# Performance work log

Measured on AMD Instinct MI355X. Metric: run time of the kernel, lower is better.

Reference implementation:

```python
import jax, jax.numpy as jnp
import numpy as np

B, LQ, LF, NW, NFR, E, D, V = 4, 128, 64, 2, 8, 128, 128, 64


def _project(x, W, b):
    # torch Emb_Projection('linear'): Linear then zero-row mask
    y = x @ W + b
    m = 1.0 - jnp.all(y == 0, axis=-1, keepdims=True).astype(y.dtype)
    return y * m


def setup_inputs() -> dict:
    key = jax.random.key(0)
    ks = jax.random.split(key, 12)
    s = lambda k, shape, fan: jax.random.normal(k, shape, jnp.float32) / np.sqrt(fan)
    return {
        "query": jax.random.normal(ks[0], (B, LQ, E), jnp.float32),
        "fragment": jax.random.normal(ks[1], (B, NW, NFR, LF, E), jnp.float32),
        "query_mask": jnp.ones((B, LQ), jnp.float32),
        "fragment_mask": jnp.ones((B, NW, NFR, LF), jnp.float32),
        # learned params (stored [in, out]; torch Linear is x @ W.T with W [out,in])
        "proj_W": s(ks[2], (E, D), E),
        "proj_b": jnp.zeros((D,), jnp.float32),
        "self_att_W": s(ks[3], (NW, D), D),   # n_way Linear(D,1,bias=False)
        "q_att_W": s(ks[4], (D, V), D),
        "f_att_W": s(ks[5], (D, V), D),
        "qf_att_W": s(ks[6], (D, V), D),
        "gate_w": s(ks[7], (V,), V),          # value_gate: Linear(V,1,bias=False)
        "val_w": s(ks[8], (V,), V),           # value_att:  Linear(V,1,bias=False)
    }


def reference(query, fragment, query_mask, fragment_mask, proj_W, proj_b,
              self_att_W, q_att_W, f_att_W, qf_att_W, gate_w, val_w):
    query = _project(query, proj_W, proj_b)          # [B,Lq,D]
    fragment = _project(fragment, proj_W, proj_b)    # [B,NW,NFR,Lf,D]

    # (1) fragment self-attention -> frag_code
    logits = jnp.einsum('bwfld,wd->bwfl', fragment, self_att_W)   # per-way Linear(D,1)
    e = jnp.exp(logits) * fragment_mask
    frag_self_att = e / (e.sum(-1, keepdims=True) + 1e-7)          # [B,NW,NFR,Lf]
    frag_code = (fragment * frag_self_att[..., None]).sum(-2)     # [B,NW,NFR,D]

    # (2) query-to-fragment attention
    frag_r = fragment.reshape(fragment.shape[0], -1, fragment.shape[-2], fragment.shape[-1])  # [B,NF,Lf,D]
    qr = query[:, None]                                            # [B,1,Lq,D]
    q_att = qr @ q_att_W                                           # [B,1,Lq,V]
    f_att = frag_r @ f_att_W                                       # [B,NF,Lf,V]
    # large broadcast product [B,NF,Lf,Lq,D] then project to V
    qf = (qr[:, :, None, :, :] * frag_r[:, :, :, None, :]) @ qf_att_W  # [B,NF,Lf,Lq,V]
    qf = q_att[:, :, None] + f_att[:, :, :, None] + qf
    qf = qf.max(axis=-3)                                           # max over Lf -> [B,NF,Lq,V]

    qf_gate = jax.nn.sigmoid(qf @ gate_w) * query_mask[:, None]    # [B,NF,Lq]
    e2 = jnp.exp(qf @ val_w) * query_mask[:, None]
    qf_norm = e2 / (e2.sum(-1, keepdims=True) + 1e-7)              # [B,NF,Lq]

    query_code = (qr * qf_norm[..., None]).sum(axis=2)             # [B,NF,D]
    query_code = query_code.reshape(frag_code.shape)               # [B,NW,NFR,D]
    return frag_code, query_code, frag_self_att, qf_gate, query
```

## Files before the change

kernel.cpp:

```cpp
#include <hip/hip_runtime.h>
#include <hip/hip_bf16.h>

#define B_   4
#define LQ_  128
#define LF_  64
#define NW_  2
#define NFR_ 8
#define E_   128
#define D_   128
#define V_   64
#define NWF_ (NW_*NFR_)

using bf16 = __hip_bfloat16;
typedef unsigned short u16;
typedef unsigned int   u32;
typedef __attribute__((ext_vector_type(8))) short  bf16x8;
typedef __attribute__((ext_vector_type(4))) float  f32x4;
typedef __attribute__((ext_vector_type(4))) u32    u32x4;

#define WS_PWT   0
#define WS_QAT   8192
#define WS_W3T   12288
#define WS_WFT   16384
#define WS_E2    20480
#define WS_QPB   28672

#define OUT_FRAGCODE  0
#define OUT_QUERYCODE 8192
#define OUT_SELFATT   16384
#define OUT_QFGATE    20480
#define OUT_QUERY     28672

#define L_FP   0
#define L_QP   16384
#define L_FA   24576
#define L_QAT  33792
#define L_SAW  38400
#define L_ATT  38912
#define L_RED  39168
#define L_TOT  41216

__device__ __forceinline__ float us2f(u16 v) { return __uint_as_float((u32)v << 16); }
__device__ __forceinline__ float lo2f(u32 v) { return __uint_as_float(v << 16); }
__device__ __forceinline__ float hi2f(u32 v) { return __uint_as_float(v & 0xffff0000u); }
__device__ __forceinline__ u16 f2b_raw(float f) {
    u32 u = __float_as_uint(f);
    return (u16)((u + 0x7fffu + ((u >> 16) & 1u)) >> 16);
}
__device__ __forceinline__ u32 pk2(float hi, float lo) {
    return __builtin_amdgcn_perm(__float_as_uint(hi), __float_as_uint(lo), 0x07060302u);
}
template<bool BF> __device__ __forceinline__ float LD(const void* p, int i) {
    return BF ? us2f(((const u16*)p)[i]) : ((const float*)p)[i];
}
template<bool BF> __device__ __forceinline__ void ST(void* p, int i, float v) {
    if (BF) ((u16*)p)[i] = f2b_raw(v); else ((float*)p)[i] = v;
}
template<bool BF> __device__ __forceinline__ u16 LDB(const void* p, int i) {
    return BF ? ((const u16*)p)[i] : f2b_raw(((const float*)p)[i]);
}
__device__ __forceinline__ bool is_bf(const void* qmask) {
    return ((const u16*)qmask)[0] == 0x3F80u;
}
template<bool BF>
__device__ __forceinline__ bf16x8 loadA(const void* x, int row, int kt, int quad) {
    int off = row * 128 + kt * 32 + quad * 8;
    if (BF) return *(const bf16x8*)((const u16*)x + off);
    f32x4 a = *(const f32x4*)((const float*)x + off);
    f32x4 c = *(const f32x4*)((const float*)x + off + 4);
    u32x4 av;
    av.x = pk2(a.y, a.x); av.y = pk2(a.w, a.z);
    av.z = pk2(c.y, c.x); av.w = pk2(c.w, c.z);
    return __builtin_bit_cast(bf16x8, av);
}

template<bool BF>
__device__ __forceinline__ void prep_body(const void* src, u16* dst, u16* stg,
                                          int N, int k0)
{
    int t = threadIdx.x, st = N + 1, total = 32 * N;
    for (int i = t; i < total; i += 256) {
        int k = i / N, v = i % N;
        stg[k * st + v] = LDB<BF>(src, (k0 + k) * N + v);
    }
    __syncthreads();
    for (int j = t; j < total; j += 256) {
        int n = j >> 5, kk = j & 31;
        dst[n * 128 + k0 + kk] = stg[kk * st + n];
    }
}
__global__ __launch_bounds__(256) void k_prep(
    const void* projW, const void* qattW, const void* qfW, const void* fattW,
    const void* qmask, float* ws)
{
    __shared__ u16 stg[32 * 129];
    int mat = blockIdx.x >> 2, kq = blockIdx.x & 3;
    const void* src = (mat == 0) ? projW : (mat == 1) ? qattW : (mat == 2) ? qfW : fattW;
    u16* dst = (u16*)(ws + ((mat == 0) ? WS_PWT : (mat == 1) ? WS_QAT : (mat == 2) ? WS_W3T : WS_WFT));
    int N = (mat == 0) ? 128 : 64;
    if (is_bf(qmask)) prep_body<true >(src, dst, stg, N, kq * 32);
    else              prep_body<false>(src, dst, stg, N, kq * 32);
}

template<bool BF>
__device__ __forceinline__ void main_body(
    const void* query, const void* fragment, const void* qmask, const void* fmask,
    const void* projB, const void* saW, const void* gatew, const void* valw,
    float* ws, void* out, char* smem)
{
    u16*   s_fp  = (u16*)(smem + L_FP);
    u16*   s_qp  = (u16*)(smem + L_QP);
    u16*   s_fa  = (u16*)(smem + L_FA);
    u16*   s_qat = (u16*)(smem + L_QAT);
    float* s_saw = (float*)(smem + L_SAW);
    float* s_att = (float*)(smem + L_ATT);
    float* s_red = (float*)(smem + L_RED);

    int bx = blockIdx.x;
    int qt = bx >> 6, bwf = bx & 63, b = bwf >> 4;
    int t = threadIdx.x, lane = t & 63, w = t >> 6;
    int m = lane & 15, quad = lane >> 4;
    int sk = (m & 7) << 3;
    const u16* pwt = (const u16*)(ws + WS_PWT);
    const u16* qatw = (const u16*)(ws + WS_QAT);
    const u16* w3t = (const u16*)(ws + WS_W3T);
    const u16* wft = (const u16*)(ws + WS_WFT);
    bool do_fragatt = (qt == (bwf & 3));
    bool do_export  = ((bwf & 15) == 0);

    if (w < 4) {
        bf16x8 afr[4];
        #pragma unroll
        for (int kt = 0; kt < 4; ++kt)
            afr[kt] = loadA<BF>(fragment, bwf * 64 + w * 16 + m, kt, quad);
        #pragma unroll
        for (int nt = 0; nt < 8; ++nt) {
            int n = nt * 16 + m;
            float bv = LD<BF>(projB, n);
            f32x4 acc = (f32x4){bv, bv, bv, bv};
            #pragma unroll
            for (int kt = 0; kt < 4; ++kt) {
                bf16x8 bw = *(const bf16x8*)(pwt + n * 128 + kt * 32 + quad * 8);
                acc = __builtin_amdgcn_mfma_f32_16x16x32_bf16(afr[kt], bw, acc, 0, 0, 0);
            }
            #pragma unroll
            for (int rr = 0; rr < 4; ++rr) {
                int row = w * 16 + quad * 4 + rr;
                s_fp[row * 128 + (n ^ ((row & 7) << 3))] = f2b_raw(acc[rr]);
            }
        }
    } else if (w < 6) {
        int q0 = (w - 4) * 16;
        bf16x8 afq[4];
        #pragma unroll
        for (int kt = 0; kt < 4; ++kt)
            afq[kt] = loadA<BF>(query, b * 128 + qt * 32 + q0 + m, kt, quad);
        #pragma unroll
        for (int nt = 0; nt < 8; ++nt) {
            int n = nt * 16 + m;
            float bv = LD<BF>(projB, n);
            f32x4 acc = (f32x4){bv, bv, bv, bv};
            #pragma unroll
            for (int kt = 0; kt < 4; ++kt) {
                bf16x8 bw = *(const bf16x8*)(pwt + n * 128 + kt * 32 + quad * 8);
                acc = __builtin_amdgcn_mfma_f32_16x16x32_bf16(afq[kt], bw, acc, 0, 0, 0);
            }
            #pragma unroll
            for (int rr = 0; rr < 4; ++rr) {
                int row = q0 + quad * 4 + rr;
                s_qp[row * 128 + (n ^ ((row & 7) << 3))] = f2b_raw(acc[rr]);
            }
        }
    }
    __syncthreads();

    if (w < 4) {
        bf16x8 afa[4];
        #pragma unroll
        for (int kt = 0; kt < 4; ++kt)
            afa[kt] = *(const bf16x8*)&s_fp[(w * 16 + m) * 128 + ((kt * 32 + quad * 8) ^ sk)];
        #pragma unroll
        for (int vt = 0; vt < 4; ++vt) {
            f32x4 a0 = (f32x4){0.f, 0.f, 0.f, 0.f};
            #pragma unroll
            for (int kt = 0; kt < 4; ++kt) {
                bf16x8 wk = *(const bf16x8*)(wft + (vt * 16 + m) * 128 + kt * 32 + quad * 8);
                a0 = __builtin_amdgcn_mfma_f32_16x16x32_bf16(afa[kt], wk, a0, 0, 0, 0);
            }
            #pragma unroll
            for (int r = 0; r < 4; ++r)
                s_fa[(w * 16 + quad * 4 + r) * 72 + vt * 16 + m] = f2b_raw(a0[r]);
        }
    } else if (w < 6) {
        int q0 = (w - 4) * 16;
        bf16x8 aq[4];
        #pragma unroll
        for (int kt = 0; kt < 4; ++kt)
            aq[kt] = *(const bf16x8*)&s_qp[(q0 + m) * 128 + ((kt * 32 + quad * 8) ^ sk)];
        #pragma unroll
        for (int vt = 0; vt < 4; ++vt) {
            f32x4 a0 = (f32x4){0.f, 0.f, 0.f, 0.f};
            #pragma unroll
            for (int kt = 0; kt < 4; ++kt) {
                bf16x8 bk = *(const bf16x8*)(qatw + (vt * 16 + m) * 128 + kt * 32 + quad * 8);
                a0 = __builtin_amdgcn_mfma_f32_16x16x32_bf16(aq[kt], bk, a0, 0, 0, 0);
            }
            #pragma unroll
            for (int r = 0; r < 4; ++r)
                s_qat[(q0 + quad * 4 + r) * 72 + vt * 16 + m] = f2b_raw(a0[r]);
        }
    }
    __syncthreads();

    int qsub = w & 1, lhalf = (w >> 1) & 1, vhalf = (w >> 2) & 1;
    bf16x8 w3f[2][4];
    #pragma unroll
    for (int i = 0; i < 2; ++i)
        #pragma unroll
        for (int kt = 0; kt < 4; ++kt)
            w3f[i][kt] = *(const bf16x8*)(w3t + ((vhalf * 2 + i) * 16 + m) * 128 + kt * 32 + quad * 8);
    float qpreg[4][8];
    {
        #pragma unroll
        for (int kt = 0; kt < 4; ++kt) {
            bf16x8 aq2 = *(const bf16x8*)&s_qp[(qsub * 16 + m) * 128 + ((kt * 32 + quad * 8) ^ sk)];
            u32x4 uv = __builtin_bit_cast(u32x4, aq2);
            qpreg[kt][0] = lo2f(uv.x); qpreg[kt][1] = hi2f(uv.x);
            qpreg[kt][2] = lo2f(uv.y); qpreg[kt][3] = hi2f(uv.y);
            qpreg[kt][4] = lo2f(uv.z); qpreg[kt][5] = hi2f(uv.z);
            qpreg[kt][6] = lo2f(uv.w); qpreg[kt][7] = hi2f(uv.w);
        }
    }
    float mx[2][4];
    #pragma unroll
    for (int i = 0; i < 2; ++i)
        #pragma unroll
        for (int r = 0; r < 4; ++r) mx[i][r] = -1e30f;

    int lbase = lhalf * 32;
    #pragma unroll 2
    for (int li = 0; li < 32; ++li) {
        int l = lbase + li;
        int sw = (l & 7) << 3;
        bf16x8 af[4];
        #pragma unroll
        for (int kt = 0; kt < 4; ++kt) {
            u32x4 fv = *(const u32x4*)&s_fp[l * 128 + ((kt * 32 + quad * 8) ^ sw)];
            u32x4 av;
            av.x = pk2(qpreg[kt][1] * hi2f(fv.x), qpreg[kt][0] * lo2f(fv.x));
            av.y = pk2(qpreg[kt][3] * hi2f(fv.y), qpreg[kt][2] * lo2f(fv.y));
            av.z = pk2(qpreg[kt][5] * hi2f(fv.z), qpreg[kt][4] * lo2f(fv.z));
            av.w = pk2(qpreg[kt][7] * hi2f(fv.w), qpreg[kt][6] * lo2f(fv.w));
            af[kt] = __builtin_bit_cast(bf16x8, av);
        }
        #pragma unroll
        for (int i = 0; i < 2; ++i) {
            float fa = us2f(s_fa[l * 72 + (vhalf * 2 + i) * 16 + m]);
            f32x4 acc = (f32x4){fa, fa, fa, fa};
            #pragma unroll
            for (int kt = 0; kt < 4; ++kt)
                acc = __builtin_amdgcn_mfma_f32_16x16x32_bf16(af[kt], w3f[i][kt], acc, 0, 0, 0);
            #pragma unroll
            for (int r = 0; r < 4; ++r) mx[i][r] = fmaxf(mx[i][r], acc[r]);
        }
    }
    __syncthreads();
    #pragma unroll
    for (int i = 0; i < 2; ++i)
        #pragma unroll
        for (int r = 0; r < 4; ++r)
            s_fa[(lhalf * 32 + qsub * 16 + quad * 4 + r) * 72 + (vhalf * 2 + i) * 16 + m] = f2b_raw(mx[i][r]);
    __syncthreads();

    {
        int q = t >> 4, vg = t & 15;
        int gq = qt * 32 + q;
        float gp = 0.f, ep = 0.f;
        #pragma unroll
        for (int jj = 0; jj < 4; ++jj) {
            int v = vg * 4 + jj;
            float mval = fmaxf(us2f(s_fa[q * 72 + v]), us2f(s_fa[(32 + q) * 72 + v]));
            float qf = mval + us2f(s_qat[q * 72 + v]);
            gp += qf * LD<BF>(gatew, v);
            ep += qf * LD<BF>(valw, v);
        }
        #pragma unroll
        for (int off = 1; off <= 8; off <<= 1) {
            gp += __shfl_xor(gp, off, 64);
            ep += __shfl_xor(ep, off, 64);
        }
        if (vg == 0) {
            float qm = LD<BF>(qmask, b * 128 + gq);
            float g = (1.0f / (1.0f + expf(-gp))) * qm;
            ST<BF>(out, OUT_QFGATE + bwf * LQ_ + gq, g);
            ws[WS_E2 + bwf * 128 + gq] = expf(ep) * qm;
        }
    }

    if (do_export) {
        u16* qpb = (u16*)(ws + WS_QPB);
        #pragma unroll
        for (int it = 0; it < 8; ++it) {
            int i = t + 512 * it;
            int row = i >> 7, col = i & 127;
            u16 raw = s_qp[row * 128 + (col ^ ((row & 7) << 3))];
            int gr = b * 128 + qt * 32 + row;
            ST<BF>(out, OUT_QUERY + gr * 128 + col, us2f(raw));
            qpb[gr * 128 + col] = raw;
        }
    }

    if (do_fragatt) {
        if (t < 128) s_saw[t] = LD<BF>(saW, ((bwf >> 3) & 1) * 128 + t);
        __syncthreads();
        {
            int l = t >> 3, j8 = t & 7;
            int swz = (l & 7) << 3;
            float p = 0.f;
            #pragma unroll
            for (int seg = 0; seg < 2; ++seg) {
                int koff = j8 * 16 + seg * 8;
                u32x4 fv = *(const u32x4*)&s_fp[l * 128 + (koff ^ swz)];
                const float* swp = &s_saw[koff];
                p += lo2f(fv.x) * swp[0] + hi2f(fv.x) * swp[1]
                   + lo2f(fv.y) * swp[2] + hi2f(fv.y) * swp[3]
                   + lo2f(fv.z) * swp[4] + hi2f(fv.z) * swp[5]
                   + lo2f(fv.w) * swp[6] + hi2f(fv.w) * swp[7];
            }
            p += __shfl_xor(p, 1, 64);
            p += __shfl_xor(p, 2, 64);
            p += __shfl_xor(p, 4, 64);
            if (j8 == 0) s_att[l] = expf(p) * LD<BF>(fmask, bwf * LF_ + l);
        }
        __syncthreads();
        if (t < 64) {
            float e = s_att[t], s = e;
            #pragma unroll
            for (int off = 1; off <= 32; off <<= 1) s += __shfl_xor(s, off, 64);
            float nrm = e / (s + 1e-7f);
            s_att[t] = nrm;
            ST<BF>(out, OUT_SELFATT + bwf * LF_ + t, nrm);
        }
        __syncthreads();
        {
            int d = t & 127, grp = t >> 7;
            float fc = 0.f;
            #pragma unroll
            for (int li2 = 0; li2 < 16; ++li2) {
                int l2 = grp * 16 + li2;
                fc += us2f(s_fp[l2 * 128 + (d ^ ((l2 & 7) << 3))]) * s_att[l2];
            }
            s_red[grp * 128 + d] = fc;
        }
        __syncthreads();
        if (t < 128)
            ST<BF>(out, OUT_FRAGCODE + bwf * D_ + t,
                   s_red[t] + s_red[128 + t] + s_red[256 + t] + s_red[384 + t]);
    }
}
__global__ __launch_bounds__(512, 4) void k_main(
    const void* query, const void* fragment, const void* qmask, const void* fmask,
    const void* projB, const void* saW, const void* gatew, const void* valw,
    float* ws, void* out)
{
    __shared__ char smem[L_TOT];
    if (is_bf(qmask))
        main_body<true >(query, fragment, qmask, fmask, projB, saW, gatew, valw, ws, out, smem);
    else
        main_body<false>(query, fragment, qmask, fmask, projB, saW, gatew, valw, ws, out, smem);
}

template<bool BF>
__device__ __forceinline__ void qcode_body(const float* ws, void* out,
                                           u16* s_q, float* s_n, float* s_part)
{
    int bwf = blockIdx.x, b = bwf >> 4, t = threadIdx.x;
    {
        const u32* src = (const u32*)((const u16*)(ws + WS_QPB) + (size_t)b * 16384);
        u32* dst = (u32*)s_q;
        #pragma unroll
        for (int it = 0; it < 64; ++it) dst[t + 128 * it] = src[t + 128 * it];
    }
    float e = ws[WS_E2 + bwf * 128 + t];
    float s = e;
    #pragma unroll
    for (int off = 1; off <= 32; off <<= 1) s += __shfl_xor(s, off, 64);
    if ((t & 63) == 0) s_part[t >> 6] = s;
    __syncthreads();
    float tot = s_part[0] + s_part[1] + 1e-7f;
    s_n[t] = e / tot;
    __syncthreads();
    float qc = 0.f;
    #pragma unroll 8
    for (int q = 0; q < 128; ++q)
        qc += us2f(s_q[q * 128 + t]) * s_n[q];
    ST<BF>(out, OUT_QUERYCODE + bwf * D_ + t, qc);
}
__global__ __launch_bounds__(128) void k_qcode(const void* qmask, const float* ws, void* out)
{
    __shared__ u16 s_q[128 * 128];
    __shared__ float s_n[128];
    __shared__ float s_part[2];
    if (is_bf(qmask)) qcode_body<true >(ws, out, s_q, s_n, s_part);
    else              qcode_body<false>(ws, out, s_q, s_n, s_part);
}

extern "C" void kernel_launch(void* const* d_in, const int* in_sizes, int n_in,
                              void* d_out, int out_size, void* d_ws, size_t ws_size,
                              hipStream_t stream)
{
    const void* query    = d_in[0];
    const void* fragment = d_in[1];
    const void* qmask    = d_in[2];
    const void* fmask    = d_in[3];
    const void* projW    = d_in[4];
    const void* projB    = d_in[5];
    const void* saW      = d_in[6];
    const void* qattW    = d_in[7];
    const void* fattW    = d_in[8];
    const void* qfW      = d_in[9];
    const void* gatew    = d_in[10];
    const void* valw     = d_in[11];
    float* ws = (float*)d_ws;

    hipLaunchKernelGGL(k_prep, dim3(16), dim3(256), 0, stream,
                       projW, qattW, qfW, fattW, qmask, ws);
    hipLaunchKernelGGL(k_main, dim3(256), dim3(512), 0, stream,
                       query, fragment, qmask, fmask, projB, saW, gatew, valw, ws, d_out);
    hipLaunchKernelGGL(k_qcode, dim3(B_ * NWF_), dim3(128), 0, stream,
                       qmask, ws, d_out);
}
```

Before: 110.9 us.

## Fuse query_code reduction into main kernel via atomic partial sums

Removes the separate k_qcode launch. Each main block now computes an unnormalized partial query_code over its 32 query rows plus the partial exp sum, and adds both atomically into a workspace accumulator that k_prep zeroes. A per-fragment counter picks the last of the four blocks, which normalizes and writes the output. This saves a kernel launch and the round trip of the projected query and e2 through global memory, at the cost of atomics, an extra block-wide sync and a threadfence in the main kernel.

```diff
diff --git a/kernel.cpp b/kernel.cpp
--- a/kernel.cpp
+++ b/kernel.cpp
@@ -22,8 +22,9 @@
 #define WS_QAT   8192
 #define WS_W3T   12288
 #define WS_WFT   16384
-#define WS_E2    20480
-#define WS_QPB   28672
+#define WS_ACC   20480
+#define WS_CNT   28928
+#define WS_ZTOT  8512
 
 #define OUT_FRAGCODE  0
 #define OUT_QUERYCODE 8192
@@ -38,7 +39,10 @@
 #define L_SAW  38400
 #define L_ATT  38912
 #define L_RED  39168
-#define L_TOT  41216
+#define L_E2   41216
+#define L_FLG  41344
+#define L_ES   41348
+#define L_TOT  41360
 
 __device__ __forceinline__ float us2f(u16 v) { return __uint_as_float((u32)v << 16); }
 __device__ __forceinline__ float lo2f(u32 v) { return __uint_as_float(v << 16); }
@@ -94,7 +98,14 @@
     const void* qmask, float* ws)
 {
     __shared__ u16 stg[32 * 129];
-    int mat = blockIdx.x >> 2, kq = blockIdx.x & 3;
+    int bx = blockIdx.x;
+    {
+        int per = (WS_ZTOT + 15) / 16;
+        int base = WS_ACC + bx * per;
+        for (int i = threadIdx.x; i < per; i += 256)
+            if (bx * per + i < WS_ZTOT) ws[base + i] = 0.f;
+    }
+    int mat = bx >> 2, kq = bx & 3;
     const void* src = (mat == 0) ? projW : (mat == 1) ? qattW : (mat == 2) ? qfW : fattW;
     u16* dst = (u16*)(ws + ((mat == 0) ? WS_PWT : (mat == 1) ? WS_QAT : (mat == 2) ? WS_W3T : WS_WFT));
     int N = (mat == 0) ? 128 : 64;
@@ -115,6 +126,9 @@
     float* s_saw = (float*)(smem + L_SAW);
     float* s_att = (float*)(smem + L_ATT);
     float* s_red = (float*)(smem + L_RED);
+    float* s_e2  = (float*)(smem + L_E2);
+    int*   s_flg = (int*)(smem + L_FLG);
+    float* s_es  = (float*)(smem + L_ES);
 
     int bx = blockIdx.x;
     int qt = bx >> 6, bwf = bx & 63, b = bwf >> 4;
@@ -293,12 +307,41 @@
             float qm = LD<BF>(qmask, b * 128 + gq);
             float g = (1.0f / (1.0f + expf(-gp))) * qm;
             ST<BF>(out, OUT_QFGATE + bwf * LQ_ + gq, g);
-            ws[WS_E2 + bwf * 128 + gq] = expf(ep) * qm;
-        }
+            s_e2[q] = expf(ep) * qm;
+        }
+    }
+    __syncthreads();
+
+    {
+        float* acc = ws + WS_ACC + bwf * 132;
+        if (t < 128) {
+            float qc = 0.f;
+            #pragma unroll
+            for (int q = 0; q < 32; ++q)
+                qc += us2f(s_qp[q * 128 + (t ^ ((q & 7) << 3))]) * s_e2[q];
+            atomicAdd(&acc[t], qc);
+        } else if (t == 128) {
+            float es = 0.f;
+            #pragma unroll
+            for (int q = 0; q < 32; ++q) es += s_e2[q];
+            atomicAdd(&acc[128], es);
+        }
+        __threadfence();
+        __syncthreads();
+        if (t == 0) *s_flg = atomicAdd((int*)(ws + WS_CNT) + bwf, 1);
+        __syncthreads();
+        bool last = (*s_flg == 3);
+        float qcv = 0.f;
+        if (last) {
+            if (t < 128) qcv = atomicAdd(&acc[t], 0.f);
+            if (t == 0)  *s_es = atomicAdd(&acc[128], 0.f);
+        }
+        __syncthreads();
+        if (last && t < 128)
+            ST<BF>(out, OUT_QUERYCODE + bwf * D_ + t, qcv / (*s_es + 1e-7f));
     }
 
     if (do_export) {
-        u16* qpb = (u16*)(ws + WS_QPB);
         #pragma unroll
         for (int it = 0; it < 8; ++it) {
             int i = t + 512 * it;
@@ -306,7 +349,6 @@
             u16 raw = s_qp[row * 128 + (col ^ ((row & 7) << 3))];
             int gr = b * 128 + qt * 32 + row;
             ST<BF>(out, OUT_QUERY + gr * 128 + col, us2f(raw));
-            qpb[gr * 128 + col] = raw;
         }
     }
 
@@ -368,41 +410,6 @@
         main_body<true >(query, fragment, qmask, fmask, projB, saW, gatew, valw, ws, out, smem);
     else
         main_body<false>(query, fragment, qmask, fmask, projB, saW, gatew, valw, ws, out, smem);
-}
-
-template<bool BF>
-__device__ __forceinline__ void qcode_body(const float* ws, void* out,
-                                           u16* s_q, float* s_n, float* s_part)
-{
-    int bwf = blockIdx.x, b = bwf >> 4, t = threadIdx.x;
-    {
-        const u32* src = (const u32*)((const u16*)(ws + WS_QPB) + (size_t)b * 16384);
-        u32* dst = (u32*)s_q;
-        #pragma unroll
-        for (int it = 0; it < 64; ++it) dst[t + 128 * it] = src[t + 128 * it];
-    }
-    float e = ws[WS_E2 + bwf * 128 + t];
-    float s = e;
-    #pragma unroll
-    for (int off = 1; off <= 32; off <<= 1) s += __shfl_xor(s, off, 64);
-    if ((t & 63) == 0) s_part[t >> 6] = s;
-    __syncthreads();
-    float tot = s_part[0] + s_part[1] + 1e-7f;
-    s_n[t] = e / tot;
-    __syncthreads();
-    float qc = 0.f;
-    #pragma unroll 8
-    for (int q = 0; q < 128; ++q)
-        qc += us2f(s_q[q * 128 + t]) * s_n[q];
-    ST<BF>(out, OUT_QUERYCODE + bwf * D_ + t, qc);
-}
-__global__ __launch_bounds__(128) void k_qcode(const void* qmask, const float* ws, void* out)
-{
-    __shared__ u16 s_q[128 * 128];
-    __shared__ float s_n[128];
-    __shared__ float s_part[2];
-    if (is_bf(qmask)) qcode_body<true >(ws, out, s_q, s_n, s_part);
-    else              qcode_body<false>(ws, out, s_q, s_n, s_part);
 }
 
 extern "C" void kernel_launch(void* const* d_in, const int* in_sizes, int n_in,
@@ -427,6 +434,4 @@
                        projW, qattW, qfW, fattW, qmask, ws);
     hipLaunchKernelGGL(k_main, dim3(256), dim3(512), 0, stream,
                        query, fragment, qmask, fmask, projB, saW, gatew, valw, ws, d_out);
-    hipLaunchKernelGGL(k_qcode, dim3(B_ * NWF_), dim3(128), 0, stream,
-                       qmask, ws, d_out);
-}
+}
```

New measurement: 138.3 us. 24.8% more time.
